# Kernel tuning notes

Measured on AMD Instinct MI355X. Metric: run time of the kernel, lower is better.

The kernel has to match this reference:

```python
import jax, jax.numpy as jnp
import numpy as np

B, NX, NY = 4, 16384, 16384
CX = CY = 256
CK = CV = 256
H = 8


def setup_inputs() -> dict:
    key = jax.random.key(0)
    ks = jax.random.split(key, 12)
    s = 0.02
    return {
        "x": jax.random.normal(ks[0], (B, NX, CX), jnp.float32),
        "y": jax.random.normal(ks[1], (B, NY, CY), jnp.float32),
        "x_pos_embed": jax.random.normal(ks[2], (B, NX, CX), jnp.float32),
        "y_pos_embed": jax.random.normal(ks[3], (B, NY, CY), jnp.float32),
        "Wq": jax.random.normal(ks[4], (CK, CX), jnp.float32) * s,
        "bq": jnp.zeros((CK,), jnp.float32),
        "Wk": jax.random.normal(ks[5], (CK, CY), jnp.float32) * s,
        "bk": jnp.zeros((CK,), jnp.float32),
        "Wv": jax.random.normal(ks[6], (CV, CY), jnp.float32) * s,
        "bv": jnp.zeros((CV,), jnp.float32),
        "Wr": jax.random.normal(ks[7], (CX, CV), jnp.float32) * s,
        "br": jnp.zeros((CX,), jnp.float32),
    }


def reference(x, y, x_pos_embed, y_pos_embed, Wq, bq, Wk, bk, Wv, bv, Wr, br):
    # Linear projections (nn.Linear: x @ W.T + b)
    q = (x + x_pos_embed) @ Wq.T + bq            # [B, Nx, Ck]
    k = (y + y_pos_embed) @ Wk.T + bk            # [B, Ny, Ck]
    v = y @ Wv.T + bv                            # [B, Ny, Cv]

    dk, dv = CK // H, CV // H
    # Split heads: [B, N, H, d] -> [B, H, N, d]
    q = q.reshape(B, NX, H, dk).transpose(0, 2, 1, 3)
    k = k.reshape(B, NY, H, dk).transpose(0, 2, 1, 3)
    v = v.reshape(B, NY, H, dv).transpose(0, 2, 1, 3)

    # key softmax over tokens (Ny); query softmax over per-head channels (dk)
    k = jax.nn.softmax(k, axis=2)                # [B, H, Ny, dk]
    q = jax.nn.softmax(q, axis=3)                # [B, H, Nx, dk]

    # context = softmax(K)^T V : [B, H, dk, dv]
    context = jnp.einsum('bhnk,bhnv->bhkv', k, v)
    # attended = Q context : [B, H, Nx, dv]
    attended = jnp.einsum('bhnk,bhkv->bhnv', q, context)

    # merge heads -> [B, Nx, Cv], reproject -> [B, Nx, Cx]
    agg = attended.transpose(0, 2, 1, 3).reshape(B, NX, CV)
    return agg @ Wr.T + br
```

## Files before the change

### kernel.cpp

```cpp
#include <hip/hip_runtime.h>


typedef float f32x4 __attribute__((ext_vector_type(4)));
typedef short s16x4 __attribute__((ext_vector_type(4)));
typedef short s16x8 __attribute__((ext_vector_type(8)));

#define MFMA16(A, B, C) __builtin_amdgcn_mfma_f32_16x16x32_bf16((A), (B), (C), 0, 0, 0)

__device__ __forceinline__ short f2bf(float f) {
    __bf16 h = (__bf16)f;
    return __builtin_bit_cast(short, h);
}
__device__ __forceinline__ float bf2f(short b) {
    unsigned u = ((unsigned)(unsigned short)b) << 16;
    return __builtin_bit_cast(float, u);
}
__device__ __forceinline__ f32x4 ntld4f(const float* p) {
    return __builtin_nontemporal_load((const f32x4*)p);
}
__device__ __forceinline__ s16x8 ntld8s(const short* p) {
    return __builtin_nontemporal_load((const s16x8*)p);
}
__device__ __forceinline__ void ntst8s(short* p, s16x8 v) {
    __builtin_nontemporal_store(v, (s16x8*)p);
}
__device__ __forceinline__ void ntst4f(float* p, f32x4 v) {
    __builtin_nontemporal_store(v, (f32x4*)p);
}

__global__ __launch_bounds__(256) void wcvt_kernel(
    const float* __restrict__ wq, const float* __restrict__ wk,
    const float* __restrict__ wv, const float* __restrict__ wr,
    short* __restrict__ wbf)
{
    int id = blockIdx.x * 256 + threadIdx.x;
    int m = id >> 13;
    int slot = id & 8191;
    int tile = slot >> 9;
    int ks   = (slot >> 6) & 7;
    int lane = slot & 63;
    int lrow = lane & 15, lgrp = lane >> 4;
    const float* src = (m == 0) ? wq : (m == 1) ? wk : (m == 2) ? wv : wr;
    const float* p = src + (size_t)(tile * 16 + lrow) * 256 + ks * 32 + lgrp * 8;
    f32x4 a = *(const f32x4*)p;
    f32x4 b = *(const f32x4*)(p + 4);
    s16x8 o;
    o[0]=f2bf(a[0]); o[1]=f2bf(a[1]); o[2]=f2bf(a[2]); o[3]=f2bf(a[3]);
    o[4]=f2bf(b[0]); o[5]=f2bf(b[1]); o[6]=f2bf(b[2]); o[7]=f2bf(b[3]);
    *(s16x8*)(wbf + (size_t)id * 8) = o;
}

__global__ __launch_bounds__(256, 4) void kv_kernel(
    const float* __restrict__ y, const float* __restrict__ ypos,
    const short* __restrict__ wkp, const short* __restrict__ wvp,
    const float* __restrict__ bk, const float* __restrict__ bv,
    short* __restrict__ e_buf, short* __restrict__ v_buf)
{
    __shared__ short smem[32 * 512];
    short* ak = smem;
    short* av = smem + 32 * 256;
    const int row0 = blockIdx.x * 32;
    const int t = threadIdx.x;
    const int w = t >> 6, lane = t & 63;

    {
        #pragma unroll
        for (int it = 0; it < 8; ++it) {
            int r = it * 4 + w;
            f32x4 a = ntld4f(y    + (size_t)(row0 + r) * 256 + lane * 4);
            f32x4 p = ntld4f(ypos + (size_t)(row0 + r) * 256 + lane * 4);
            f32x4 k = a + p;
            s16x4 ov, ok;
            ov[0]=f2bf(a[0]); ov[1]=f2bf(a[1]); ov[2]=f2bf(a[2]); ov[3]=f2bf(a[3]);
            ok[0]=f2bf(k[0]); ok[1]=f2bf(k[1]); ok[2]=f2bf(k[2]); ok[3]=f2bf(k[3]);
            int swz = ((lane >> 1) ^ (r & 7)) * 8 + (lane & 1) * 4;
            *(s16x4*)(av + r * 256 + swz) = ov;
            *(s16x4*)(ak + r * 256 + swz) = ok;
        }
    }
    __syncthreads();

    const int lrow = lane & 15, lgrp = lane >> 4;
    const bool is_k = (w < 2);
    const int colbase = (w & 1) * 128;
    const int tile0 = colbase >> 4;
    const short* WP = is_k ? wkp : wvp;
    const float* bp = is_k ? bk : bv;
    const short* A = is_k ? ak : av;

    float bias[8];
    #pragma unroll
    for (int nf = 0; nf < 8; ++nf) bias[nf] = bp[colbase + nf * 16 + lrow];

    s16x8 af[2][8];
    #pragma unroll
    for (int mf = 0; mf < 2; ++mf) {
        int rr = mf * 16 + lrow;
        #pragma unroll
        for (int ks = 0; ks < 8; ++ks) {
            int cs = ((ks * 4 + lgrp) ^ (rr & 7));
            af[mf][ks] = *(const s16x8*)(A + rr * 256 + cs * 8);
        }
    }
    __syncthreads();

    #pragma unroll
    for (int nf = 0; nf < 8; ++nf) {
        const int tile = tile0 + nf;
        const short* wt = WP + ((size_t)tile * 8) * 512 + lane * 8;
        f32x4 a0 = (f32x4){0.f, 0.f, 0.f, 0.f};
        f32x4 a1 = (f32x4){0.f, 0.f, 0.f, 0.f};
        #pragma unroll
        for (int kg = 0; kg < 2; ++kg) {
            s16x8 bf[4];
            #pragma unroll
            for (int kk = 0; kk < 4; ++kk)
                bf[kk] = *(const s16x8*)(wt + (kg * 4 + kk) * 512);
            #pragma unroll
            for (int kk = 0; kk < 4; ++kk) {
                a0 = MFMA16(af[0][kg * 4 + kk], bf[kk], a0);
                a1 = MFMA16(af[1][kg * 4 + kk], bf[kk], a1);
            }
        }
        const int colp = (is_k ? 0 : 256) + colbase + nf * 16 + lrow;
        #pragma unroll
        for (int rr = 0; rr < 4; ++rr) {
            float v0 = a0[rr] + bias[nf];
            float v1 = a1[rr] + bias[nf];
            if (is_k) { v0 = __expf(v0); v1 = __expf(v1); }
            int lr0 = lgrp * 4 + rr;
            int lr1 = lr0 + 16;
            smem[lr0 * 512 + (((colp >> 3) ^ (lr0 & 7)) * 8) + (colp & 7)] = f2bf(v0);
            smem[lr1 * 512 + (((colp >> 3) ^ (lr1 & 7)) * 8) + (colp & 7)] = f2bf(v1);
        }
    }
    __syncthreads();

    {
        #pragma unroll
        for (int i = 0; i < 8; ++i) {
            int r = i * 4 + w;
            int grow = row0 + r;
            s16x8 val = *(const s16x8*)(smem + r * 512 + ((lane ^ (r & 7)) << 3));
            if (lane < 32)
                ntst8s(e_buf + (size_t)grow * 256 + lane * 8, val);
            else
                ntst8s(v_buf + (size_t)grow * 256 + (lane - 32) * 8, val);
        }
    }
}

__global__ __launch_bounds__(256) void ctx_kernel(
    const short* __restrict__ e_buf, const short* __restrict__ v_buf,
    float* __restrict__ partials)
{
    __shared__ float se[128 * 32];
    __shared__ float sv[128 * 32];
    __shared__ float red[4 * 1056];
    const int cb = blockIdx.x, bh = blockIdx.y;
    const int b = bh >> 3, h = bh & 7;
    const int tok0 = b * 16384 + cb * 512;
    const int t = threadIdx.x, w = t >> 6, lane = t & 63;
    const int ckb = (lane >> 3) * 4, cvb = (lane & 7) * 4;

    f32x4 acc[4];
    #pragma unroll
    for (int i = 0; i < 4; ++i) acc[i] = (f32x4){0.f, 0.f, 0.f, 0.f};
    f32x4 dn = (f32x4){0.f, 0.f, 0.f, 0.f};

    for (int it = 0; it < 4; ++it) {
        __syncthreads();
        #pragma unroll
        for (int s = 0; s < 2; ++s) {
            int id = t + s * 256;
            int rr = id >> 2, pp = id & 3;
            size_t g = (size_t)(tok0 + it * 128 + rr) * 256 + h * 32 + pp * 8;
            s16x8 ee = ntld8s(e_buf + g);
            s16x8 vv = ntld8s(v_buf + g);
            f32x4 e0 = {bf2f(ee[0]), bf2f(ee[1]), bf2f(ee[2]), bf2f(ee[3])};
            f32x4 e1 = {bf2f(ee[4]), bf2f(ee[5]), bf2f(ee[6]), bf2f(ee[7])};
            f32x4 v0 = {bf2f(vv[0]), bf2f(vv[1]), bf2f(vv[2]), bf2f(vv[3])};
            f32x4 v1 = {bf2f(vv[4]), bf2f(vv[5]), bf2f(vv[6]), bf2f(vv[7])};
            *(f32x4*)(se + rr * 32 + pp * 8)     = e0;
            *(f32x4*)(se + rr * 32 + pp * 8 + 4) = e1;
            *(f32x4*)(sv + rr * 32 + pp * 8)     = v0;
            *(f32x4*)(sv + rr * 32 + pp * 8 + 4) = v1;
        }
        __syncthreads();
        const int r0 = w * 32;
        #pragma unroll 8
        for (int rr = 0; rr < 32; ++rr) {
            f32x4 e4 = *(const f32x4*)(se + (r0 + rr) * 32 + ckb);
            f32x4 v4 = *(const f32x4*)(sv + (r0 + rr) * 32 + cvb);
            acc[0] += e4[0] * v4;
            acc[1] += e4[1] * v4;
            acc[2] += e4[2] * v4;
            acc[3] += e4[3] * v4;
            dn += e4;
        }
    }
    __syncthreads();
    #pragma unroll
    for (int i = 0; i < 4; ++i)
        *(f32x4*)(red + w * 1056 + (ckb + i) * 32 + cvb) = acc[i];
    if ((lane & 7) == 0)
        *(f32x4*)(red + w * 1056 + 1024 + ckb) = dn;
    __syncthreads();
    float* outp = partials + (size_t)(bh * 32 + cb) * 1056;
    for (int e = t; e < 1056; e += 256)
        outp[e] = red[e] + red[1056 + e] + red[2112 + e] + red[3168 + e];
}

__global__ __launch_bounds__(256) void ctxred2_kernel(
    const float* __restrict__ partials, const float* __restrict__ wr,
    short* __restrict__ mpk)
{
    __shared__ float s[1056];
    const int bh = blockIdx.x, t = threadIdx.x;
    const int b = bh >> 3, h = bh & 7;
    for (int e = t; e < 1056; e += 256) {
        float a = 0.f;
        #pragma unroll 4
        for (int c = 0; c < 32; ++c) a += partials[(size_t)(bh * 32 + c) * 1056 + e];
        s[e] = a;
    }
    __syncthreads();
    for (int e = t; e < 1024; e += 256)
        s[e] = s[e] / s[1024 + (e >> 5)];
    __syncthreads();

    #pragma unroll 4
    for (int i = 0; i < 32; ++i) {
        int linear = i * 256 + t;
        int tile = linear >> 9, rem = linear & 511;
        int lane = rem >> 3, j = rem & 7;
        int col = tile * 16 + (lane & 15);
        int ck = (lane >> 4) * 8 + j;
        const float* wrow = wr + (size_t)col * 256 + h * 32;
        const float* cr = s + ck * 32;
        float m = 0.f;
        #pragma unroll
        for (int dv = 0; dv < 32; dv += 4) {
            f32x4 wv = *(const f32x4*)(wrow + dv);
            m += cr[dv] * wv[0] + cr[dv + 1] * wv[1]
               + cr[dv + 2] * wv[2] + cr[dv + 3] * wv[3];
        }
        mpk[(((size_t)(b * 16 + tile)) * 8 + h) * 512 + rem] = f2bf(m);
    }
}

__global__ __launch_bounds__(256) void qout_kernel(
    const float* __restrict__ x, const float* __restrict__ xpos,
    const short* __restrict__ wqp, const float* __restrict__ bq,
    const short* __restrict__ mpk, const float* __restrict__ br,
    float* __restrict__ out)
{
    __shared__ short smem[32 * 512];
    short* alds = smem;
    const int row0 = blockIdx.x * 32;
    const int b = row0 >> 14;
    const int t = threadIdx.x;
    const int w = t >> 6, lane = t & 63;

    {
        f32x4 lx[8], lp[8];
        #pragma unroll
        for (int it = 0; it < 8; ++it) {
            int r = it * 4 + w;
            lx[it] = ntld4f(x    + (size_t)(row0 + r) * 256 + lane * 4);
            lp[it] = ntld4f(xpos + (size_t)(row0 + r) * 256 + lane * 4);
        }
        #pragma unroll
        for (int it = 0; it < 8; ++it) {
            int r = it * 4 + w;
            f32x4 a = lx[it] + lp[it];
            s16x4 o;
            o[0]=f2bf(a[0]); o[1]=f2bf(a[1]); o[2]=f2bf(a[2]); o[3]=f2bf(a[3]);
            int swz = ((lane >> 1) ^ (r & 7)) * 8 + (lane & 1) * 4;
            *(s16x4*)(alds + r * 256 + swz) = o;
        }
    }
    __syncthreads();

    const int lrow = lane & 15, lgrp = lane >> 4;
    const int wc = w * 64;
    const int tile0 = wc >> 4;

    float biasq[4];
    #pragma unroll
    for (int nf = 0; nf < 4; ++nf) biasq[nf] = bq[wc + nf * 16 + lrow];

    f32x4 acc[2][4];
    #pragma unroll
    for (int mf = 0; mf < 2; ++mf)
        #pragma unroll
        for (int nf = 0; nf < 4; ++nf) acc[mf][nf] = (f32x4){0.f, 0.f, 0.f, 0.f};

    {
        const short* wq8 = wqp + lane * 8;
        s16x8 bfq[2][4];
        #pragma unroll
        for (int nf = 0; nf < 4; ++nf)
            bfq[0][nf] = *(const s16x8*)(wq8 + ((size_t)(tile0 + nf) * 8 + 0) * 512);
        #pragma unroll
        for (int ks = 0; ks < 8; ++ks) {
            const int cur = ks & 1, nxt = cur ^ 1;
            if (ks < 7) {
                #pragma unroll
                for (int nf = 0; nf < 4; ++nf)
                    bfq[nxt][nf] = *(const s16x8*)(wq8 + ((size_t)(tile0 + nf) * 8 + ks + 1) * 512);
            }
            s16x8 af[2];
            #pragma unroll
            for (int mf = 0; mf < 2; ++mf) {
                int rr = mf * 16 + lrow;
                int cs = (ks * 4 + lgrp) ^ (rr & 7);
                af[mf] = *(const s16x8*)(alds + rr * 256 + cs * 8);
            }
            #pragma unroll
            for (int nf = 0; nf < 4; ++nf) {
                acc[0][nf] = MFMA16(af[0], bfq[cur][nf], acc[0][nf]);
                acc[1][nf] = MFMA16(af[1], bfq[cur][nf], acc[1][nf]);
            }
        }
    }
    __syncthreads();

    #pragma unroll
    for (int mf = 0; mf < 2; ++mf) {
        f32x4 e[4];
        #pragma unroll
        for (int nf = 0; nf < 4; ++nf)
            #pragma unroll
            for (int rr = 0; rr < 4; ++rr)
                e[nf][rr] = __expf(acc[mf][nf][rr] + biasq[nf]);
        #pragma unroll
        for (int hl = 0; hl < 2; ++hl) {
            #pragma unroll
            for (int rr = 0; rr < 4; ++rr) {
                float s = e[hl * 2][rr] + e[hl * 2 + 1][rr];
                s += __shfl_xor(s, 1);
                s += __shfl_xor(s, 2);
                s += __shfl_xor(s, 4);
                s += __shfl_xor(s, 8);
                float rinv = 1.0f / s;
                int row = mf * 16 + lgrp * 4 + rr;
                #pragma unroll
                for (int n2 = 0; n2 < 2; ++n2) {
                    int col = wc + hl * 32 + n2 * 16 + lrow;
                    int cs = (col >> 3) ^ (row & 7);
                    alds[row * 256 + cs * 8 + (col & 7)] = f2bf(e[hl * 2 + n2][rr] * rinv);
                }
            }
        }
    }
    __syncthreads();

    float biasr[4];
    #pragma unroll
    for (int nf = 0; nf < 4; ++nf) biasr[nf] = br[wc + nf * 16 + lrow];

    f32x4 acc2[2][4];
    #pragma unroll
    for (int mf = 0; mf < 2; ++mf)
        #pragma unroll
        for (int nf = 0; nf < 4; ++nf) acc2[mf][nf] = (f32x4){0.f, 0.f, 0.f, 0.f};

    {
        const short* mp8 = mpk + (size_t)b * 65536 + lane * 8;
        s16x8 bfr[2][4];
        #pragma unroll
        for (int nf = 0; nf < 4; ++nf)
            bfr[0][nf] = *(const s16x8*)(mp8 + ((size_t)(tile0 + nf) * 8 + 0) * 512);
        #pragma unroll
        for (int ks = 0; ks < 8; ++ks) {
            const int cur = ks & 1, nxt = cur ^ 1;
            if (ks < 7) {
                #pragma unroll
                for (int nf = 0; nf < 4; ++nf)
                    bfr[nxt][nf] = *(const s16x8*)(mp8 + ((size_t)(tile0 + nf) * 8 + ks + 1) * 512);
            }
            s16x8 af[2];
            #pragma unroll
            for (int mf = 0; mf < 2; ++mf) {
                int rr = mf * 16 + lrow;
                int cs = (ks * 4 + lgrp) ^ (rr & 7);
                af[mf] = *(const s16x8*)(alds + rr * 256 + cs * 8);
            }
            #pragma unroll
            for (int nf = 0; nf < 4; ++nf) {
                acc2[0][nf] = MFMA16(af[0], bfr[cur][nf], acc2[0][nf]);
                acc2[1][nf] = MFMA16(af[1], bfr[cur][nf], acc2[1][nf]);
            }
        }
    }
    __syncthreads();

    float* cf = (float*)smem;
    #pragma unroll
    for (int mf = 0; mf < 2; ++mf)
      #pragma unroll
      for (int nf = 0; nf < 4; ++nf)
        #pragma unroll
        for (int rr = 0; rr < 4; ++rr) {
            int row = mf * 16 + lgrp * 4 + rr;
            int col = wc + nf * 16 + lrow;
            int chunk = col >> 2, pos = col & 3;
            cf[row * 256 + ((chunk ^ (row & 7)) << 2) + pos] = acc2[mf][nf][rr] + biasr[nf];
        }
    __syncthreads();

    #pragma unroll
    for (int i = 0; i < 8; ++i) {
        int r = i * 4 + w;
        f32x4 val = *(const f32x4*)(cf + r * 256 + (((lane ^ (r & 7)) & 63) << 2));
        ntst4f(out + (size_t)(row0 + r) * 256 + lane * 4, val);
    }
}

extern "C" void kernel_launch(void* const* d_in, const int* in_sizes, int n_in,
                              void* d_out, int out_size, void* d_ws, size_t ws_size,
                              hipStream_t stream)
{
    const float* x    = (const float*)d_in[0];
    const float* y    = (const float*)d_in[1];
    const float* xpos = (const float*)d_in[2];
    const float* ypos = (const float*)d_in[3];
    const float* Wq   = (const float*)d_in[4];
    const float* bq   = (const float*)d_in[5];
    const float* Wk   = (const float*)d_in[6];
    const float* bk   = (const float*)d_in[7];
    const float* Wv   = (const float*)d_in[8];
    const float* bv   = (const float*)d_in[9];
    const float* Wr   = (const float*)d_in[10];
    const float* br   = (const float*)d_in[11];

    char*  ws    = (char*)d_ws;
    short* wbf   = (short*)(ws);
    short* mpk   = (short*)(ws + 524288);
    float* parts = (float*)(ws + (1 << 20));
    short* e_buf = (short*)(ws + ((size_t)6 << 20));
    short* v_buf = e_buf + (size_t)65536 * 256;
    float* outp  = (float*)d_out;

    hipLaunchKernelGGL(wcvt_kernel, dim3(128), dim3(256), 0, stream,
                       Wq, Wk, Wv, Wr, wbf);
    hipLaunchKernelGGL(kv_kernel, dim3(2048), dim3(256), 0, stream,
                       y, ypos, wbf + 65536, wbf + 131072, bk, bv, e_buf, v_buf);
    hipLaunchKernelGGL(ctx_kernel, dim3(32, 32), dim3(256), 0, stream,
                       e_buf, v_buf, parts);
    hipLaunchKernelGGL(ctxred2_kernel, dim3(32), dim3(256), 0, stream,
                       parts, Wr, mpk);
    hipLaunchKernelGGL(qout_kernel, dim3(2048), dim3(256), 0, stream,
                       x, xpos, wbf, bq, mpk, br, outp);
}
```

Measured before the change: 175.8 us.

## Merge Q projection and softmax into the KV kernel, split output projection

After: 191.9 us. 1.09x slower.

```diff
diff --git a/kernel.cpp b/kernel.cpp
--- a/kernel.cpp
+++ b/kernel.cpp
@@ -50,20 +50,25 @@
     *(s16x8*)(wbf + (size_t)id * 8) = o;
 }
 
-__global__ __launch_bounds__(256, 4) void kv_kernel(
+__global__ __launch_bounds__(256) void fused_kernel(
     const float* __restrict__ y, const float* __restrict__ ypos,
     const short* __restrict__ wkp, const short* __restrict__ wvp,
     const float* __restrict__ bk, const float* __restrict__ bv,
-    short* __restrict__ e_buf, short* __restrict__ v_buf)
+    short* __restrict__ e_buf, short* __restrict__ v_buf,
+    const float* __restrict__ x, const float* __restrict__ xpos,
+    const short* __restrict__ wqp, const float* __restrict__ bq,
+    short* __restrict__ qsm, int qsm_base)
 {
     __shared__ short smem[32 * 512];
-    short* ak = smem;
-    short* av = smem + 32 * 256;
-    const int row0 = blockIdx.x * 32;
     const int t = threadIdx.x;
     const int w = t >> 6, lane = t & 63;
-
-    {
+    const int lrow = lane & 15, lgrp = lane >> 4;
+
+    if ((int)blockIdx.x < qsm_base) {
+        short* ak = smem;
+        short* av = smem + 32 * 256;
+        const int row0 = blockIdx.x * 32;
+
         #pragma unroll
         for (int it = 0; it < 8; ++it) {
             int r = it * 4 + w;
@@ -77,66 +82,63 @@
             *(s16x4*)(av + r * 256 + swz) = ov;
             *(s16x4*)(ak + r * 256 + swz) = ok;
         }
-    }
-    __syncthreads();
-
-    const int lrow = lane & 15, lgrp = lane >> 4;
-    const bool is_k = (w < 2);
-    const int colbase = (w & 1) * 128;
-    const int tile0 = colbase >> 4;
-    const short* WP = is_k ? wkp : wvp;
-    const float* bp = is_k ? bk : bv;
-    const short* A = is_k ? ak : av;
-
-    float bias[8];
-    #pragma unroll
-    for (int nf = 0; nf < 8; ++nf) bias[nf] = bp[colbase + nf * 16 + lrow];
-
-    s16x8 af[2][8];
-    #pragma unroll
-    for (int mf = 0; mf < 2; ++mf) {
-        int rr = mf * 16 + lrow;
-        #pragma unroll
-        for (int ks = 0; ks < 8; ++ks) {
-            int cs = ((ks * 4 + lgrp) ^ (rr & 7));
-            af[mf][ks] = *(const s16x8*)(A + rr * 256 + cs * 8);
-        }
-    }
-    __syncthreads();
-
-    #pragma unroll
-    for (int nf = 0; nf < 8; ++nf) {
-        const int tile = tile0 + nf;
-        const short* wt = WP + ((size_t)tile * 8) * 512 + lane * 8;
-        f32x4 a0 = (f32x4){0.f, 0.f, 0.f, 0.f};
-        f32x4 a1 = (f32x4){0.f, 0.f, 0.f, 0.f};
-        #pragma unroll
-        for (int kg = 0; kg < 2; ++kg) {
-            s16x8 bf[4];
-            #pragma unroll
-            for (int kk = 0; kk < 4; ++kk)
-                bf[kk] = *(const s16x8*)(wt + (kg * 4 + kk) * 512);
-            #pragma unroll
-            for (int kk = 0; kk < 4; ++kk) {
-                a0 = MFMA16(af[0][kg * 4 + kk], bf[kk], a0);
-                a1 = MFMA16(af[1][kg * 4 + kk], bf[kk], a1);
-            }
-        }
-        const int colp = (is_k ? 0 : 256) + colbase + nf * 16 + lrow;
-        #pragma unroll
-        for (int rr = 0; rr < 4; ++rr) {
-            float v0 = a0[rr] + bias[nf];
-            float v1 = a1[rr] + bias[nf];
-            if (is_k) { v0 = __expf(v0); v1 = __expf(v1); }
-            int lr0 = lgrp * 4 + rr;
-            int lr1 = lr0 + 16;
-            smem[lr0 * 512 + (((colp >> 3) ^ (lr0 & 7)) * 8) + (colp & 7)] = f2bf(v0);
-            smem[lr1 * 512 + (((colp >> 3) ^ (lr1 & 7)) * 8) + (colp & 7)] = f2bf(v1);
-        }
-    }
-    __syncthreads();
-
-    {
+        __syncthreads();
+
+        const bool is_k = (w < 2);
+        const int colbase = (w & 1) * 128;
+        const int tile0 = colbase >> 4;
+        const short* WP = is_k ? wkp : wvp;
+        const float* bp = is_k ? bk : bv;
+        const short* A = is_k ? ak : av;
+
+        float bias[8];
+        #pragma unroll
+        for (int nf = 0; nf < 8; ++nf) bias[nf] = bp[colbase + nf * 16 + lrow];
+
+        s16x8 af[2][8];
+        #pragma unroll
+        for (int mf = 0; mf < 2; ++mf) {
+            int rr = mf * 16 + lrow;
+            #pragma unroll
+            for (int ks = 0; ks < 8; ++ks) {
+                int cs = ((ks * 4 + lgrp) ^ (rr & 7));
+                af[mf][ks] = *(const s16x8*)(A + rr * 256 + cs * 8);
+            }
+        }
+        __syncthreads();
+
+        #pragma unroll
+        for (int nf = 0; nf < 8; ++nf) {
+            const int tile = tile0 + nf;
+            const short* wt = WP + ((size_t)tile * 8) * 512 + lane * 8;
+            f32x4 a0 = (f32x4){0.f, 0.f, 0.f, 0.f};
+            f32x4 a1 = (f32x4){0.f, 0.f, 0.f, 0.f};
+            #pragma unroll
+            for (int kg = 0; kg < 2; ++kg) {
+                s16x8 bf[4];
+                #pragma unroll
+                for (int kk = 0; kk < 4; ++kk)
+                    bf[kk] = *(const s16x8*)(wt + (kg * 4 + kk) * 512);
+                #pragma unroll
+                for (int kk = 0; kk < 4; ++kk) {
+                    a0 = MFMA16(af[0][kg * 4 + kk], bf[kk], a0);
+                    a1 = MFMA16(af[1][kg * 4 + kk], bf[kk], a1);
+                }
+            }
+            const int colp = (is_k ? 0 : 256) + colbase + nf * 16 + lrow;
+            #pragma unroll
+            for (int rr = 0; rr < 4; ++rr) {
+                float v0 = a0[rr] + bias[nf];
+                float v1 = a1[rr] + bias[nf];
+                if (is_k) { v0 = __expf(v0); v1 = __expf(v1); }
+                int lr0 = lgrp * 4 + rr;
+                int lr1 = lr0 + 16;
+                smem[lr0 * 512 + (((colp >> 3) ^ (lr0 & 7)) * 8) + (colp & 7)] = f2bf(v0);
+                smem[lr1 * 512 + (((colp >> 3) ^ (lr1 & 7)) * 8) + (colp & 7)] = f2bf(v1);
+            }
+        }
+        __syncthreads();
+
         #pragma unroll
         for (int i = 0; i < 8; ++i) {
             int r = i * 4 + w;
@@ -146,6 +148,110 @@
                 ntst8s(e_buf + (size_t)grow * 256 + lane * 8, val);
             else
                 ntst8s(v_buf + (size_t)grow * 256 + (lane - 32) * 8, val);
+        }
+    } else {
+        short* alds = smem;
+        const int blk = blockIdx.x - qsm_base;
+        const int row0 = blk * 32;
+
+        {
+            f32x4 lx[8], lp[8];
+            #pragma unroll
+            for (int it = 0; it < 8; ++it) {
+                int r = it * 4 + w;
+                lx[it] = ntld4f(x    + (size_t)(row0 + r) * 256 + lane * 4);
+                lp[it] = ntld4f(xpos + (size_t)(row0 + r) * 256 + lane * 4);
+            }
+            #pragma unroll
+            for (int it = 0; it < 8; ++it) {
+                int r = it * 4 + w;
+                f32x4 a = lx[it] + lp[it];
+                s16x4 o;
+                o[0]=f2bf(a[0]); o[1]=f2bf(a[1]); o[2]=f2bf(a[2]); o[3]=f2bf(a[3]);
+                int swz = ((lane >> 1) ^ (r & 7)) * 8 + (lane & 1) * 4;
+                *(s16x4*)(alds + r * 256 + swz) = o;
+            }
+        }
+        __syncthreads();
+
+        const int wc = w * 64;
+        const int tile0 = wc >> 4;
+
+        float biasq[4];
+        #pragma unroll
+        for (int nf = 0; nf < 4; ++nf) biasq[nf] = bq[wc + nf * 16 + lrow];
+
+        f32x4 acc[2][4];
+        #pragma unroll
+        for (int mf = 0; mf < 2; ++mf)
+            #pragma unroll
+            for (int nf = 0; nf < 4; ++nf) acc[mf][nf] = (f32x4){0.f, 0.f, 0.f, 0.f};
+
+        {
+            const short* wq8 = wqp + lane * 8;
+            s16x8 bfq[2][4];
+            #pragma unroll
+            for (int nf = 0; nf < 4; ++nf)
+                bfq[0][nf] = *(const s16x8*)(wq8 + ((size_t)(tile0 + nf) * 8 + 0) * 512);
+            #pragma unroll
+            for (int ks = 0; ks < 8; ++ks) {
+                const int cur = ks & 1, nxt = cur ^ 1;
+                if (ks < 7) {
+                    #pragma unroll
+                    for (int nf = 0; nf < 4; ++nf)
+                        bfq[nxt][nf] = *(const s16x8*)(wq8 + ((size_t)(tile0 + nf) * 8 + ks + 1) * 512);
+                }
+                s16x8 af[2];
+                #pragma unroll
+                for (int mf = 0; mf < 2; ++mf) {
+                    int rr = mf * 16 + lrow;
+                    int cs = (ks * 4 + lgrp) ^ (rr & 7);
+                    af[mf] = *(const s16x8*)(alds + rr * 256 + cs * 8);
+                }
+                #pragma unroll
+                for (int nf = 0; nf < 4; ++nf) {
+                    acc[0][nf] = MFMA16(af[0], bfq[cur][nf], acc[0][nf]);
+                    acc[1][nf] = MFMA16(af[1], bfq[cur][nf], acc[1][nf]);
+                }
+            }
+        }
+        __syncthreads();
+
+        #pragma unroll
+        for (int mf = 0; mf < 2; ++mf) {
+            f32x4 e[4];
+            #pragma unroll
+            for (int nf = 0; nf < 4; ++nf)
+                #pragma unroll
+                for (int rr = 0; rr < 4; ++rr)
+                    e[nf][rr] = __expf(acc[mf][nf][rr] + biasq[nf]);
+            #pragma unroll
+            for (int hl = 0; hl < 2; ++hl) {
+                #pragma unroll
+                for (int rr = 0; rr < 4; ++rr) {
+                    float s = e[hl * 2][rr] + e[hl * 2 + 1][rr];
+                    s += __shfl_xor(s, 1);
+                    s += __shfl_xor(s, 2);
+                    s += __shfl_xor(s, 4);
+                    s += __shfl_xor(s, 8);
+                    float rinv = 1.0f / s;
+                    int row = mf * 16 + lgrp * 4 + rr;
+                    #pragma unroll
+                    for (int n2 = 0; n2 < 2; ++n2) {
+                        int col = wc + hl * 32 + n2 * 16 + lrow;
+                        int cs = (col >> 3) ^ (row & 7);
+                        alds[row * 256 + cs * 8 + (col & 7)] = f2bf(e[hl * 2 + n2][rr] * rinv);
+                    }
+                }
+            }
+        }
+        __syncthreads();
+
+        short* qb = qsm + (size_t)blk * 8192;
+        #pragma unroll
+        for (int i = 0; i < 4; ++i) {
+            s16x8 v = *(const s16x8*)(smem + i * 2048 + t * 8);
+            ntst8s(qb + i * 2048 + t * 8, v);
         }
     }
 }
@@ -246,6 +352,92 @@
                + cr[dv + 2] * wv[2] + cr[dv + 3] * wv[3];
         }
         mpk[(((size_t)(b * 16 + tile)) * 8 + h) * 512 + rem] = f2bf(m);
+    }
+}
+
+__global__ __launch_bounds__(256) void out2_kernel(
+    const short* __restrict__ qsm, const short* __restrict__ mpk,
+    const float* __restrict__ br, float* __restrict__ out)
+{
+    __shared__ short smem[32 * 512];
+    short* alds = smem;
+    const int row0 = blockIdx.x * 32;
+    const int b = row0 >> 14;
+    const int t = threadIdx.x;
+    const int w = t >> 6, lane = t & 63;
+    const int lrow = lane & 15, lgrp = lane >> 4;
+    const int wc = w * 64;
+    const int tile0 = wc >> 4;
+
+    {
+        const short* qb = qsm + (size_t)blockIdx.x * 8192;
+        #pragma unroll
+        for (int i = 0; i < 4; ++i) {
+            s16x8 v = ntld8s(qb + i * 2048 + t * 8);
+            *(s16x8*)(smem + i * 2048 + t * 8) = v;
+        }
+    }
+    __syncthreads();
+
+    float biasr[4];
+    #pragma unroll
+    for (int nf = 0; nf < 4; ++nf) biasr[nf] = br[wc + nf * 16 + lrow];
+
+    f32x4 acc2[2][4];
+    #pragma unroll
+    for (int mf = 0; mf < 2; ++mf)
+        #pragma unroll
+        for (int nf = 0; nf < 4; ++nf) acc2[mf][nf] = (f32x4){0.f, 0.f, 0.f, 0.f};
+
+    {
+        const short* mp8 = mpk + (size_t)b * 65536 + lane * 8;
+        s16x8 bfr[2][4];
+        #pragma unroll
+        for (int nf = 0; nf < 4; ++nf)
+            bfr[0][nf] = *(const s16x8*)(mp8 + ((size_t)(tile0 + nf) * 8 + 0) * 512);
+        #pragma unroll
+        for (int ks = 0; ks < 8; ++ks) {
+            const int cur = ks & 1, nxt = cur ^ 1;
+            if (ks < 7) {
+                #pragma unroll
+                for (int nf = 0; nf < 4; ++nf)
+                    bfr[nxt][nf] = *(const s16x8*)(mp8 + ((size_t)(tile0 + nf) * 8 + ks + 1) * 512);
+            }
+            s16x8 af[2];
+            #pragma unroll
+            for (int mf = 0; mf < 2; ++mf) {
+                int rr = mf * 16 + lrow;
+                int cs = (ks * 4 + lgrp) ^ (rr & 7);
+                af[mf] = *(const s16x8*)(alds + rr * 256 + cs * 8);
+            }
+            #pragma unroll
+            for (int nf = 0; nf < 4; ++nf) {
+                acc2[0][nf] = MFMA16(af[0], bfr[cur][nf], acc2[0][nf]);
+                acc2[1][nf] = MFMA16(af[1], bfr[cur][nf], acc2[1][nf]);
+            }
+        }
+    }
+    __syncthreads();
+
+    float* cf = (float*)smem;
+    #pragma unroll
+    for (int mf = 0; mf < 2; ++mf)
+      #pragma unroll
+      for (int nf = 0; nf < 4; ++nf)
+        #pragma unroll
+        for (int rr = 0; rr < 4; ++rr) {
+            int row = mf * 16 + lgrp * 4 + rr;
+            int col = wc + nf * 16 + lrow;
+            int chunk = col >> 2, pos = col & 3;
+            cf[row * 256 + ((chunk ^ (row & 7)) << 2) + pos] = acc2[mf][nf][rr] + biasr[nf];
+        }
+    __syncthreads();
+
+    #pragma unroll
+    for (int i = 0; i < 8; ++i) {
+        int r = i * 4 + w;
+        f32x4 val = *(const f32x4*)(cf + r * 256 + (((lane ^ (r & 7)) & 63) << 2));
+        ntst4f(out + (size_t)(row0 + r) * 256 + lane * 4, val);
     }
 }
 
@@ -441,16 +633,32 @@
     float* parts = (float*)(ws + (1 << 20));
     short* e_buf = (short*)(ws + ((size_t)6 << 20));
     short* v_buf = e_buf + (size_t)65536 * 256;
+    short* qsm   = (short*)(ws + ((size_t)74 << 20));
     float* outp  = (float*)d_out;
+
+    const bool big_ws = ws_size >= ((size_t)112 << 20);
 
     hipLaunchKernelGGL(wcvt_kernel, dim3(128), dim3(256), 0, stream,
                        Wq, Wk, Wv, Wr, wbf);
-    hipLaunchKernelGGL(kv_kernel, dim3(2048), dim3(256), 0, stream,
-                       y, ypos, wbf + 65536, wbf + 131072, bk, bv, e_buf, v_buf);
-    hipLaunchKernelGGL(ctx_kernel, dim3(32, 32), dim3(256), 0, stream,
-                       e_buf, v_buf, parts);
-    hipLaunchKernelGGL(ctxred2_kernel, dim3(32), dim3(256), 0, stream,
-                       parts, Wr, mpk);
-    hipLaunchKernelGGL(qout_kernel, dim3(2048), dim3(256), 0, stream,
-                       x, xpos, wbf, bq, mpk, br, outp);
-}
+    if (big_ws) {
+        hipLaunchKernelGGL(fused_kernel, dim3(4096), dim3(256), 0, stream,
+                           y, ypos, wbf + 65536, wbf + 131072, bk, bv, e_buf, v_buf,
+                           x, xpos, wbf, bq, qsm, 2048);
+        hipLaunchKernelGGL(ctx_kernel, dim3(32, 32), dim3(256), 0, stream,
+                           e_buf, v_buf, parts);
+        hipLaunchKernelGGL(ctxred2_kernel, dim3(32), dim3(256), 0, stream,
+                           parts, Wr, mpk);
+        hipLaunchKernelGGL(out2_kernel, dim3(2048), dim3(256), 0, stream,
+                           qsm, mpk, br, outp);
+    } else {
+        hipLaunchKernelGGL(fused_kernel, dim3(2048), dim3(256), 0, stream,
+                           y, ypos, wbf + 65536, wbf + 131072, bk, bv, e_buf, v_buf,
+                           x, xpos, wbf, bq, (short*)e_buf , 2048);
+        hipLaunchKernelGGL(ctx_kernel, dim3(32, 32), dim3(256), 0, stream,
+                           e_buf, v_buf, parts);
+        hipLaunchKernelGGL(ctxred2_kernel, dim3(32), dim3(256), 0, stream,
+                           parts, Wr, mpk);
+        hipLaunchKernelGGL(qout_kernel, dim3(2048), dim3(256), 0, stream,
+                           x, xpos, wbf, bq, mpk, br, outp);
+    }
+}
```
